# Kernel tuning notes

Measured on AMD Instinct MI355X. Metric: run time of the kernel, lower is better.

Reference implementation:

```python
import jax, jax.numpy as jnp
import numpy as np

M, N, H, C = 50000, 50000, 32, 128
K, GROUPS = 15, 8
CPG = C // GROUPS           # 16, channels per group
RADIUS, SIGMA, INF = 2.5, 1.0, 1.0e6
EPS = 1e-5                  # GroupNorm eps
NEG_SLOPE = 0.1             # LeakyReLU slope in alpha MLP


def setup_inputs() -> dict:
    key = jax.random.key(0)
    ks = jax.random.split(key, 12)
    q_pts = jax.random.normal(ks[0], (M, 3), jnp.float32) * 5.0
    s_pts = q_pts  # same-resolution layer: q == s
    s_feats = jax.random.normal(ks[1], (N, C), jnp.float32)
    neighb_inds = jax.random.randint(ks[2], (M, H), 0, N + 1)  # N = padding index
    # kernel points: center + 14 points in a sphere of given radius
    kp = jax.random.normal(ks[3], (K, 3), jnp.float32)
    kp = kp / (jnp.linalg.norm(kp, axis=1, keepdims=True) + 1e-9) * RADIUS * 0.66
    k_pts = kp.at[0].set(0.0)
    # alpha MLP: Linear(C->C) + LeakyReLU + Linear(C->K*CPG)
    W1 = jax.random.normal(ks[4], (C, C), jnp.float32) * np.sqrt(2.0 / C)
    b1 = jnp.zeros((C,), jnp.float32)
    W2 = jax.random.normal(ks[5], (C, K * CPG), jnp.float32) * np.sqrt(2.0 / C)
    b2 = jnp.zeros((K * CPG,), jnp.float32)
    gn_w = jnp.ones((K * CPG,), jnp.float32)
    gn_b = jnp.zeros((K * CPG,), jnp.float32)
    return {"q_pts": q_pts, "s_pts": s_pts, "s_feats": s_feats,
            "neighb_inds": neighb_inds, "k_pts": k_pts,
            "W1": W1, "b1": b1, "W2": W2, "b2": b2,
            "gn_w": gn_w, "gn_b": gn_b}


def reference(q_pts, s_pts, s_feats, k_pts, W1, b1, W2, b2, gn_w, gn_b, neighb_inds):
    m = q_pts.shape[0]
    # ---- neighbor geometry (no_grad in original) ----
    s_pts_pad = jnp.concatenate([s_pts, jnp.full((1, 3), INF, s_pts.dtype)], 0)
    neighbors = s_pts_pad[neighb_inds] - q_pts[:, None, :]          # (M,H,3)
    sq = jnp.sum((neighbors[:, :, None, :] - k_pts) ** 2, -1)       # (M,H,K)
    nn_sq = jnp.min(sq, -1)                                         # (M,H)
    nn_1nn = jnp.argmin(sq, -1)                                     # (M,H)
    infl = jnp.clip(1.0 - jnp.sqrt(nn_sq) / SIGMA, 0.0)             # linear influence
    # ---- neighbor features gather (padding row = zeros) ----
    feats_pad = jnp.concatenate([s_feats, jnp.zeros((1, C), s_feats.dtype)], 0)
    neighbor_feats = feats_pad[neighb_inds]                         # (M,H,C)
    # ---- dynamic weights from center features (q==s -> pooled = s_feats) ----
    pooled = s_feats
    h = pooled @ W1 + b1
    h = jnp.where(h >= 0, h, NEG_SLOPE * h)                         # LeakyReLU(0.1)
    cw = (h @ W2 + b2).reshape(m, K, CPG)                           # (M,K,CPG)
    # GroupNorm(K groups over K*CPG channels), stats over (points, CPG) per group
    mu = jnp.mean(cw, axis=(0, 2), keepdims=True)
    var = jnp.var(cw, axis=(0, 2), keepdims=True)
    cw = (cw - mu) * jax.lax.rsqrt(var + EPS)
    cw = cw * gn_w.reshape(1, K, CPG) + gn_b.reshape(1, K, CPG)
    # ---- gather weights at nearest kernel point, modulate by influence ----
    nw = jnp.take_along_axis(cw, nn_1nn[:, :, None], axis=1)        # (M,H,CPG)
    nw = nw * infl[:, :, None]                                      # weight_act = identity
    # ---- multiply and sum over neighbors ----
    nf = neighbor_feats.reshape(m, H, CPG, GROUPS)
    out = jnp.sum(nf * nw[:, :, :, None], axis=1)                   # (M,CPG,GROUPS)
    return out.reshape(m, C)
```

## Files before the change

### kernel.cpp

```cpp
#include <hip/hip_runtime.h>
#include <hip/hip_bf16.h>

#define Mpts 50000
#define Npts 50000
#define Hn 32
#define Cc 128
#define Kk 15
#define NCW 240

typedef __attribute__((ext_vector_type(8))) short short8;
typedef __attribute__((ext_vector_type(4))) float f32x4;
typedef __attribute__((ext_vector_type(2))) float f32x2;
typedef unsigned int u32;

__device__ inline ushort f2bf(float f) {
  __hip_bfloat16 h = __float2bfloat16(f);
  return *reinterpret_cast<ushort*>(&h);
}

__global__ __launch_bounds__(256) void k0_pre(
    const float* __restrict__ W1, const float* __restrict__ W2,
    ushort* __restrict__ sfb, ushort* __restrict__ W1t,
    ushort* __restrict__ W2t, float* __restrict__ stats)
{
  __shared__ ushort TT[240][66];
  const int t = threadIdx.x;
  const int b = blockIdx.x;
  if (b < 2) {
    const int k0 = b * 64;
#pragma unroll
    for (int i = 0; i < 32; ++i) {
      int e = t + i * 256;
      int r = e >> 7, c = e & 127;
      TT[c][r] = f2bf(W1[(size_t)(k0 + r) * Cc + c]);
    }
    __syncthreads();
    int n = t >> 1, half = t & 1;
    union { short8 v[4]; ushort u[32]; } pk;
#pragma unroll
    for (int i = 0; i < 32; ++i) pk.u[i] = TT[n][half * 32 + i];
#pragma unroll
    for (int q = 0; q < 4; ++q)
      *(short8*)(W1t + (size_t)n * Cc + k0 + half * 32 + q * 8) = pk.v[q];
  } else if (b < 4) {
    const int k0 = (b - 2) * 64;
    for (int i = 0; i < 60; ++i) {
      int e = t + i * 256;
      int r = e / 240, c = e % 240;
      TT[c][r] = f2bf(W2[(size_t)(k0 + r) * NCW + c]);
    }
    __syncthreads();
    if (t < 240) {
      union { short8 v[8]; ushort u[64]; } pk;
#pragma unroll
      for (int i = 0; i < 64; ++i) pk.u[i] = TT[t][i];
#pragma unroll
      for (int q = 0; q < 8; ++q)
        *(short8*)(W2t + (size_t)t * Cc + k0 + q * 8) = pk.v[q];
    }
  } else {
    if (t < 16) {
      short8 z = short8{0,0,0,0,0,0,0,0};
      *(short8*)(sfb + (size_t)Npts * Cc + t * 8) = z;
    }
    if (t < 128) {
      float4 z4 = make_float4(0.f, 0.f, 0.f, 0.f);
      *(float4*)(stats + t * 4) = z4;
    }
  }
}

__global__ __launch_bounds__(256, 3) void k1_mlp(
    const float* __restrict__ sfeat, const ushort* __restrict__ W1t,
    const float* __restrict__ b1, const ushort* __restrict__ W2t,
    const float* __restrict__ b2, ushort* __restrict__ sfb,
    ushort* __restrict__ cw, float* __restrict__ stats)
{
  __shared__ __align__(16) ushort shA[64 * 128];
  __shared__ __align__(16) ushort shW[128 * 128];
  __shared__ float red[2][15][4];

  const int t = threadIdx.x;
  const int r0 = blockIdx.x * 64;
  const int wid = t >> 6, lane = t & 63;
  const int l16 = lane & 15, lq = lane >> 4;

  float4 fA[4], fB[4];
#pragma unroll
  for (int p = 0; p < 4; ++p) {
    int id = p * 256 + t;
    int r = id >> 4, c = id & 15;
    int g = r0 + r;
    fA[p] = make_float4(0.f, 0.f, 0.f, 0.f);
    fB[p] = make_float4(0.f, 0.f, 0.f, 0.f);
    if (g < Mpts) {
      const float* src = sfeat + (size_t)g * Cc + c * 8;
      fA[p] = *(const float4*)(src);
      fB[p] = *(const float4*)(src + 4);
    }
  }
  uint4 wv[8];
#pragma unroll
  for (int p = 0; p < 8; ++p) {
    int id = p * 256 + t;
    int r = id >> 4, c = id & 15;
    wv[p] = *(const uint4*)(W1t + r * Cc + c * 8);
  }
  asm volatile("" :: "v"(wv[0].x), "v"(wv[1].x), "v"(wv[2].x), "v"(wv[3].x),
                     "v"(wv[4].x), "v"(wv[5].x), "v"(wv[6].x), "v"(wv[7].x),
                     "v"(fA[0].x), "v"(fA[1].x), "v"(fA[2].x), "v"(fA[3].x),
                     "v"(fB[0].x), "v"(fB[1].x), "v"(fB[2].x), "v"(fB[3].x));
#pragma unroll
  for (int p = 0; p < 8; ++p) {
    int id = p * 256 + t;
    int r = id >> 4, c = id & 15;
    *(uint4*)((char*)shW + ((r * 256 + c * 16) ^ ((r & 7) << 4))) = wv[p];
  }
#pragma unroll
  for (int p = 0; p < 4; ++p) {
    int id = p * 256 + t;
    int r = id >> 4, c = id & 15;
    int g = r0 + r;
    union { short8 s; ushort u[8]; } pk;
    pk.u[0] = f2bf(fA[p].x); pk.u[1] = f2bf(fA[p].y); pk.u[2] = f2bf(fA[p].z); pk.u[3] = f2bf(fA[p].w);
    pk.u[4] = f2bf(fB[p].x); pk.u[5] = f2bf(fB[p].y); pk.u[6] = f2bf(fB[p].z); pk.u[7] = f2bf(fB[p].w);
    if (g < Mpts) *(short8*)(sfb + (size_t)g * Cc + c * 8) = pk.s;
    *(short8*)((char*)shA + ((r * 256 + c * 16) ^ ((r & 7) << 4))) = pk.s;
  }
  __syncthreads();

  const int arow = wid * 16 + l16;
  const int axor = (arow & 7) << 4;

  f32x4 acc1[8];
#pragma unroll
  for (int nt = 0; nt < 8; ++nt) acc1[nt] = f32x4{0.f, 0.f, 0.f, 0.f};
#pragma unroll
  for (int kt = 0; kt < 4; ++kt) {
    const int koff2 = (kt * 32 + lq * 8) * 2;
    short8 a = *(const short8*)((const char*)shA + ((arow * 256 + koff2) ^ axor));
#pragma unroll
    for (int nt = 0; nt < 8; ++nt) {
      int wrow = nt * 16 + l16;
      short8 b = *(const short8*)((const char*)shW + ((wrow * 256 + koff2) ^ ((wrow & 7) << 4)));
      acc1[nt] = __builtin_amdgcn_mfma_f32_16x16x32_bf16(a, b, acc1[nt], 0, 0, 0);
    }
  }
#pragma unroll
  for (int nt = 0; nt < 8; ++nt) {
    int col = nt * 16 + l16;
    float bias = b1[col];
#pragma unroll
    for (int reg = 0; reg < 4; ++reg) {
      float h = acc1[nt][reg] + bias;
      h = h >= 0.f ? h : 0.1f * h;
      int row = wid * 16 + lq * 4 + reg;
      int byte = ((row * 256) + col * 2) ^ ((row & 7) << 4);
      *(ushort*)((char*)shA + byte) = f2bf(h);
    }
  }

  f32x4 acc2[8], acc3[7];
#pragma unroll
  for (int j = 0; j < 8; ++j) acc2[j] = f32x4{0.f, 0.f, 0.f, 0.f};
#pragma unroll
  for (int j = 0; j < 7; ++j) acc3[j] = f32x4{0.f, 0.f, 0.f, 0.f};

  __syncthreads();
  {
    uint4 wv2[8];
#pragma unroll
    for (int p = 0; p < 8; ++p) {
      int id = p * 256 + t;
      int r = id >> 4, c = id & 15;
      wv2[p] = *(const uint4*)(W2t + (size_t)r * Cc + c * 8);
    }
    asm volatile("" :: "v"(wv2[0].x), "v"(wv2[1].x), "v"(wv2[2].x), "v"(wv2[3].x),
                       "v"(wv2[4].x), "v"(wv2[5].x), "v"(wv2[6].x), "v"(wv2[7].x));
#pragma unroll
    for (int p = 0; p < 8; ++p) {
      int id = p * 256 + t;
      int r = id >> 4, c = id & 15;
      *(uint4*)((char*)shW + ((r * 256 + c * 16) ^ ((r & 7) << 4))) = wv2[p];
    }
  }
  __syncthreads();
#pragma unroll
  for (int kt = 0; kt < 4; ++kt) {
    const int koff2 = (kt * 32 + lq * 8) * 2;
    short8 a = *(const short8*)((const char*)shA + ((arow * 256 + koff2) ^ axor));
#pragma unroll
    for (int j = 0; j < 8; ++j) {
      int wrow = j * 16 + l16;
      short8 b = *(const short8*)((const char*)shW + ((wrow * 256 + koff2) ^ ((wrow & 7) << 4)));
      acc2[j] = __builtin_amdgcn_mfma_f32_16x16x32_bf16(a, b, acc2[j], 0, 0, 0);
    }
  }

  __syncthreads();
  {
    uint4 wv2[7];
#pragma unroll
    for (int p = 0; p < 7; ++p) {
      int id = p * 256 + t;
      int r = id >> 4, c = id & 15;
      wv2[p] = *(const uint4*)(W2t + (size_t)(128 + r) * Cc + c * 8);
    }
    asm volatile("" :: "v"(wv2[0].x), "v"(wv2[1].x), "v"(wv2[2].x), "v"(wv2[3].x),
                       "v"(wv2[4].x), "v"(wv2[5].x), "v"(wv2[6].x));
#pragma unroll
    for (int p = 0; p < 7; ++p) {
      int id = p * 256 + t;
      int r = id >> 4, c = id & 15;
      *(uint4*)((char*)shW + ((r * 256 + c * 16) ^ ((r & 7) << 4))) = wv2[p];
    }
  }
  __syncthreads();
#pragma unroll
  for (int kt = 0; kt < 4; ++kt) {
    const int koff2 = (kt * 32 + lq * 8) * 2;
    short8 a = *(const short8*)((const char*)shA + ((arow * 256 + koff2) ^ axor));
#pragma unroll
    for (int j = 0; j < 7; ++j) {
      int wrow = j * 16 + l16;
      short8 b = *(const short8*)((const char*)shW + ((wrow * 256 + koff2) ^ ((wrow & 7) << 4)));
      acc3[j] = __builtin_amdgcn_mfma_f32_16x16x32_bf16(a, b, acc3[j], 0, 0, 0);
    }
  }
  __syncthreads();

  ushort* shB = shW;
  float s[15], ss[15];
#pragma unroll
  for (int j = 0; j < 15; ++j) { s[j] = 0.f; ss[j] = 0.f; }
  const int rowb = wid * 16 + lq * 4;
#pragma unroll
  for (int j = 0; j < 15; ++j) {
    int col = j * 16 + l16;
    float bias = b2[col];
#pragma unroll
    for (int reg = 0; reg < 4; ++reg) {
      float v = (j < 8 ? acc2[j][reg] : acc3[j - 8][reg]) + bias;
      shB[(rowb + reg) * 244 + col] = f2bf(v);
      if (r0 + rowb + reg < Mpts) { s[j] += v; ss[j] += v * v; }
    }
  }
  __syncthreads();

  {
    char* cwB = (char*)cw + (size_t)r0 * 480;
#pragma unroll
    for (int i = 0; i < 8; ++i) {
      int gid = i * 256 + t;
      if (gid < 1920) {
        int row = gid / 30;
        int rem = (gid - row * 30) * 16;
        if (r0 + row < Mpts) {
          uint4 v = *(const uint4*)((const char*)shB + row * 488 + rem);
          *(uint4*)(cwB + (size_t)row * 480 + rem) = v;
        }
      }
    }
  }

#pragma unroll
  for (int j = 0; j < 15; ++j) {
    for (int off = 32; off > 0; off >>= 1) {
      s[j]  += __shfl_xor(s[j],  off);
      ss[j] += __shfl_xor(ss[j], off);
    }
  }
  if (lane == 0) {
#pragma unroll
    for (int j = 0; j < 15; ++j) { red[0][j][wid] = s[j]; red[1][j][wid] = ss[j]; }
  }
  __syncthreads();
  float* st = stats + (blockIdx.x & 7) * 64;
  if (t < 15) {
    float S = red[0][t][0] + red[0][t][1] + red[0][t][2] + red[0][t][3];
    atomicAdd(&st[t], S);
  } else if (t >= 32 && t < 47) {
    int j = t - 32;
    float SS = red[1][j][0] + red[1][j][1] + red[1][j][2] + red[1][j][3];
    atomicAdd(&st[32 + j], SS);
  }
}

__global__ __launch_bounds__(256) void k3_out(
    const float* __restrict__ q_pts, const float* __restrict__ s_pts,
    const ushort* __restrict__ sfb, const int* __restrict__ nb,
    const float* __restrict__ kp, const float* __restrict__ gn_w,
    const float* __restrict__ gn_b, const float* __restrict__ stats,
    const ushort* __restrict__ cw, float* __restrict__ out)
{
  __shared__ float Atab[255], Btab[255];
  __shared__ float mus[16], rss[16];
  __shared__ float kpt[3][15];
  __shared__ float wtab[4][2][8][33];
  const int t = threadIdx.x;

  if (t < 15) {
    float S = 0.f, SS = 0.f;
#pragma unroll
    for (int r = 0; r < 8; ++r) { S += stats[r * 64 + t]; SS += stats[r * 64 + 32 + t]; }
    const float inv = 1.0f / (16.0f * (float)Mpts);
    float mu = S * inv;
    float var = SS * inv - mu * mu;
    mus[t] = mu;
    rss[t] = rsqrtf(var + 1e-5f);
  } else if (t >= 64 && t < 109) {
    int i = t - 64;
    kpt[i % 3][i / 3] = kp[i];
  }
  __syncthreads();
  if (t < 240) {
    int k = t >> 4, c = t & 15;
    float a = rss[k] * gn_w[t];
    Atab[k * 17 + c] = a;
    Btab[k * 17 + c] = gn_b[t] - mus[k] * a;
  }
  __syncthreads();

  const int half = (blockIdx.x >= 6250) ? 1 : 0;
  const int pblk = blockIdx.x - half * 6250;
  const int wid = t >> 6, lane = t & 63;
  const int mbase = pblk * 8 + wid * 2;
  const int gtid = pblk * 256 + t;
  const int ch = lane & 7, hlane = (lane >> 3) & 3, p = lane >> 5;
  const int half8 = half * 8;

  int idxv = nb[gtid]; if (idxv > Npts) idxv = Npts;

  int ih[8];
#pragma unroll
  for (int j = 0; j < 8; ++j)
    ih[j] = __shfl(idxv, (p << 5) | (hlane + 4 * j));
  const uint4* fb = (const uint4*)sfb;
  uint4 fv[8];
#pragma unroll
  for (int j = 0; j < 8; ++j)
    fv[j] = fb[ih[j] * 16 + half8 + ch];

  u32 gpk;
  {
    const int mg = mbase + (lane >> 5);
    float qx = q_pts[mg * 3 + 0], qy = q_pts[mg * 3 + 1], qz = q_pts[mg * 3 + 2];
    float px, py, pz;
    if (idxv < Npts) { px = s_pts[idxv * 3 + 0]; py = s_pts[idxv * 3 + 1]; pz = s_pts[idxv * 3 + 2]; }
    else             { px = 1.0e6f; py = 1.0e6f; pz = 1.0e6f; }
    float nx = px - qx, ny = py - qy, nz = pz - qz;
    int ksel = 0; float best = 1e30f;
#pragma unroll
    for (int k = 0; k < Kk; ++k) {
      float dx = nx - kpt[0][k], dy = ny - kpt[1][k], dz = nz - kpt[2][k];
      float d = dx * dx + dy * dy + dz * dz;
      if (d < best) { best = d; ksel = k; }
    }
    float infl = 1.f - sqrtf(best);
    infl = infl > 0.f ? infl : 0.f;
    gpk = (__float_as_uint(infl) & 0xFFFFFFF0u) | (u32)ksel;
  }

  {
    int h = lane >> 1, c0 = (lane & 1) * 4;
#pragma unroll
    for (int q = 0; q < 2; ++q) {
      u32 gp = __shfl((int)gpk, (q << 5) | h);
      int kh = gp & 15;
      float wI = __uint_as_float(gp & 0xFFFFFFF0u);
      uint2 cwv = *(const uint2*)(cw + (size_t)(mbase + q) * NCW + kh * 16 + half8 + c0);
      const float* Ar = &Atab[kh * 17 + half8 + c0];
      const float* Br = &Btab[kh * 17 + half8 + c0];
      float v0 = __uint_as_float(cwv.x << 16);
      float v1 = __uint_as_float(cwv.x & 0xffff0000u);
      float v2 = __uint_as_float(cwv.y << 16);
      float v3 = __uint_as_float(cwv.y & 0xffff0000u);
      wtab[wid][q][c0 + 0][h] = fmaf(v0, Ar[0], Br[0]) * wI;
      wtab[wid][q][c0 + 1][h] = fmaf(v1, Ar[1], Br[1]) * wI;
      wtab[wid][q][c0 + 2][h] = fmaf(v2, Ar[2], Br[2]) * wI;
      wtab[wid][q][c0 + 3][h] = fmaf(v3, Ar[3], Br[3]) * wI;
    }
  }

  asm volatile("" :: "v"(fv[0].x), "v"(fv[1].x), "v"(fv[2].x), "v"(fv[3].x),
                     "v"(fv[4].x), "v"(fv[5].x), "v"(fv[6].x), "v"(fv[7].x));

  f32x2 a0 = {0.f, 0.f}, a1 = {0.f, 0.f}, a2 = {0.f, 0.f}, a3 = {0.f, 0.f};
#pragma unroll
  for (int j = 0; j < 8; ++j) {
    float w = wtab[wid][p][ch][hlane + 4 * j];
    f32x2 w2 = {w, w};
    u32 ux = fv[j].x, uy = fv[j].y, uz = fv[j].z, uw = fv[j].w;
    f32x2 q0 = {__uint_as_float(ux << 16), __uint_as_float(ux & 0xffff0000u)};
    f32x2 q1 = {__uint_as_float(uy << 16), __uint_as_float(uy & 0xffff0000u)};
    f32x2 q2 = {__uint_as_float(uz << 16), __uint_as_float(uz & 0xffff0000u)};
    f32x2 q3 = {__uint_as_float(uw << 16), __uint_as_float(uw & 0xffff0000u)};
    a0 = __builtin_elementwise_fma(q0, w2, a0);
    a1 = __builtin_elementwise_fma(q1, w2, a1);
    a2 = __builtin_elementwise_fma(q2, w2, a2);
    a3 = __builtin_elementwise_fma(q3, w2, a3);
  }
#pragma unroll
  for (int off = 8; off <= 16; off <<= 1) {
    a0[0] += __shfl_xor(a0[0], off); a0[1] += __shfl_xor(a0[1], off);
    a1[0] += __shfl_xor(a1[0], off); a1[1] += __shfl_xor(a1[1], off);
    a2[0] += __shfl_xor(a2[0], off); a2[1] += __shfl_xor(a2[1], off);
    a3[0] += __shfl_xor(a3[0], off); a3[1] += __shfl_xor(a3[1], off);
  }
  if ((lane & 24) == 0) {
    float* op = out + (size_t)(mbase + p) * Cc + half * 64 + ch * 8;
    float4 o0; o0.x = a0[0]; o0.y = a0[1]; o0.z = a1[0]; o0.w = a1[1];
    float4 o1; o1.x = a2[0]; o1.y = a2[1]; o1.z = a3[0]; o1.w = a3[1];
    *(float4*)(op)     = o0;
    *(float4*)(op + 4) = o1;
  }
}

extern "C" void kernel_launch(void* const* d_in, const int* in_sizes, int n_in,
                              void* d_out, int out_size, void* d_ws, size_t ws_size,
                              hipStream_t stream) {
  const float* q_pts  = (const float*)d_in[0];
  const float* s_pts  = (const float*)d_in[1];
  const float* sfeat  = (const float*)d_in[2];
  const int*   nb     = (const int*)d_in[3];
  const float* kp     = (const float*)d_in[4];
  const float* W1     = (const float*)d_in[5];
  const float* b1     = (const float*)d_in[6];
  const float* W2     = (const float*)d_in[7];
  const float* b2     = (const float*)d_in[8];
  const float* gn_w   = (const float*)d_in[9];
  const float* gn_b   = (const float*)d_in[10];
  float* out   = (float*)d_out;

  char* wsb = (char*)d_ws;
  float*  stats = (float*)wsb;
  ushort* sfb   = (ushort*)(wsb + 4096);
  ushort* W1t   = (ushort*)(wsb + 12804352);
  ushort* W2t   = (ushort*)(wsb + 12837120);
  ushort* cwb   = (ushort*)(wsb + 12898560);

  k0_pre<<<5, 256, 0, stream>>>(W1, W2, sfb, W1t, W2t, stats);
  k1_mlp<<<(Mpts + 63) / 64, 256, 0, stream>>>(sfeat, W1t, b1, W2t, b2,
                                               sfb, cwb, stats);
  k3_out<<<12500, 256, 0, stream>>>(q_pts, s_pts, sfb, nb, kp, gn_w, gn_b,
                                    stats, cwb, out);
}
```

Before: 108.6 us.

## Move neighbor geometry computation from output kernel into MLP kernel

The nearest-kernel-point search and influence computation move out of k3_out and into k1_mlp, which writes a packed per-neighbor word (influence plus kernel index) to a workspace buffer. Previously k3_out ran this work twice, once per channel half. The geometry now runs once and overlaps with the MLP kernel's tail, and k3_out only reads one u32 per neighbor. The cost is an extra 6.4 MB write and read through global memory, plus more work in k1_mlp, which may affect its occupancy.

```diff
diff --git a/kernel.cpp b/kernel.cpp
--- a/kernel.cpp
+++ b/kernel.cpp
@@ -74,16 +74,22 @@
     const float* __restrict__ sfeat, const ushort* __restrict__ W1t,
     const float* __restrict__ b1, const ushort* __restrict__ W2t,
     const float* __restrict__ b2, ushort* __restrict__ sfb,
-    ushort* __restrict__ cw, float* __restrict__ stats)
+    ushort* __restrict__ cw, float* __restrict__ stats,
+    const float* __restrict__ q_pts, const float* __restrict__ s_pts,
+    const int* __restrict__ nb, const float* __restrict__ kp,
+    u32* __restrict__ geomP)
 {
   __shared__ __align__(16) ushort shA[64 * 128];
   __shared__ __align__(16) ushort shW[128 * 128];
   __shared__ float red[2][15][4];
+  __shared__ float kptS[45];
 
   const int t = threadIdx.x;
   const int r0 = blockIdx.x * 64;
   const int wid = t >> 6, lane = t & 63;
   const int l16 = lane & 15, lq = lane >> 4;
+
+  if (t < 45) kptS[t] = kp[t];
 
   float4 fA[4], fB[4];
 #pragma unroll
@@ -263,6 +269,33 @@
     }
   }
 
+  {
+    const int gbase = blockIdx.x * 2048 + t;
+#pragma unroll
+    for (int i = 0; i < 8; ++i) {
+      int gt = gbase + i * 256;
+      if (gt < Mpts * Hn) {
+        int idx = nb[gt]; if (idx > Npts) idx = Npts;
+        int m = gt >> 5;
+        float qx = q_pts[m * 3 + 0], qy = q_pts[m * 3 + 1], qz = q_pts[m * 3 + 2];
+        float px, py, pz;
+        if (idx < Npts) { px = s_pts[idx * 3 + 0]; py = s_pts[idx * 3 + 1]; pz = s_pts[idx * 3 + 2]; }
+        else            { px = 1.0e6f; py = 1.0e6f; pz = 1.0e6f; }
+        float nx = px - qx, ny = py - qy, nz = pz - qz;
+        int ksel = 0; float best = 1e30f;
+#pragma unroll
+        for (int k = 0; k < Kk; ++k) {
+          float dx = nx - kptS[k * 3 + 0], dy = ny - kptS[k * 3 + 1], dz = nz - kptS[k * 3 + 2];
+          float d = dx * dx + dy * dy + dz * dz;
+          if (d < best) { best = d; ksel = k; }
+        }
+        float infl = 1.f - sqrtf(best);
+        infl = infl > 0.f ? infl : 0.f;
+        geomP[gt] = (__float_as_uint(infl) & 0xFFFFFFF0u) | (u32)ksel;
+      }
+    }
+  }
+
 #pragma unroll
   for (int j = 0; j < 15; ++j) {
     for (int off = 32; off > 0; off >>= 1) {
@@ -287,15 +320,13 @@
 }
 
 __global__ __launch_bounds__(256) void k3_out(
-    const float* __restrict__ q_pts, const float* __restrict__ s_pts,
     const ushort* __restrict__ sfb, const int* __restrict__ nb,
-    const float* __restrict__ kp, const float* __restrict__ gn_w,
+    const u32* __restrict__ geomP, const float* __restrict__ gn_w,
     const float* __restrict__ gn_b, const float* __restrict__ stats,
     const ushort* __restrict__ cw, float* __restrict__ out)
 {
   __shared__ float Atab[255], Btab[255];
   __shared__ float mus[16], rss[16];
-  __shared__ float kpt[3][15];
   __shared__ float wtab[4][2][8][33];
   const int t = threadIdx.x;
 
@@ -308,9 +339,6 @@
     float var = SS * inv - mu * mu;
     mus[t] = mu;
     rss[t] = rsqrtf(var + 1e-5f);
-  } else if (t >= 64 && t < 109) {
-    int i = t - 64;
-    kpt[i % 3][i / 3] = kp[i];
   }
   __syncthreads();
   if (t < 240) {
@@ -329,43 +357,22 @@
   const int ch = lane & 7, hlane = (lane >> 3) & 3, p = lane >> 5;
   const int half8 = half * 8;
 
+  u32 g = geomP[gtid];
   int idxv = nb[gtid]; if (idxv > Npts) idxv = Npts;
 
-  int ih[8];
-#pragma unroll
-  for (int j = 0; j < 8; ++j)
-    ih[j] = __shfl(idxv, (p << 5) | (hlane + 4 * j));
   const uint4* fb = (const uint4*)sfb;
   uint4 fv[8];
 #pragma unroll
-  for (int j = 0; j < 8; ++j)
-    fv[j] = fb[ih[j] * 16 + half8 + ch];
-
-  u32 gpk;
-  {
-    const int mg = mbase + (lane >> 5);
-    float qx = q_pts[mg * 3 + 0], qy = q_pts[mg * 3 + 1], qz = q_pts[mg * 3 + 2];
-    float px, py, pz;
-    if (idxv < Npts) { px = s_pts[idxv * 3 + 0]; py = s_pts[idxv * 3 + 1]; pz = s_pts[idxv * 3 + 2]; }
-    else             { px = 1.0e6f; py = 1.0e6f; pz = 1.0e6f; }
-    float nx = px - qx, ny = py - qy, nz = pz - qz;
-    int ksel = 0; float best = 1e30f;
-#pragma unroll
-    for (int k = 0; k < Kk; ++k) {
-      float dx = nx - kpt[0][k], dy = ny - kpt[1][k], dz = nz - kpt[2][k];
-      float d = dx * dx + dy * dy + dz * dz;
-      if (d < best) { best = d; ksel = k; }
-    }
-    float infl = 1.f - sqrtf(best);
-    infl = infl > 0.f ? infl : 0.f;
-    gpk = (__float_as_uint(infl) & 0xFFFFFFF0u) | (u32)ksel;
+  for (int j = 0; j < 8; ++j) {
+    int ih = __shfl(idxv, (p << 5) | (hlane + 4 * j));
+    fv[j] = fb[ih * 16 + half8 + ch];
   }
 
   {
     int h = lane >> 1, c0 = (lane & 1) * 4;
 #pragma unroll
     for (int q = 0; q < 2; ++q) {
-      u32 gp = __shfl((int)gpk, (q << 5) | h);
+      u32 gp = __shfl((int)g, (q << 5) | h);
       int kh = gp & 15;
       float wI = __uint_as_float(gp & 0xFFFFFFF0u);
       uint2 cwv = *(const uint2*)(cw + (size_t)(mbase + q) * NCW + kh * 16 + half8 + c0);
@@ -438,10 +445,12 @@
   ushort* W1t   = (ushort*)(wsb + 12804352);
   ushort* W2t   = (ushort*)(wsb + 12837120);
   ushort* cwb   = (ushort*)(wsb + 12898560);
+  u32*    geomP = (u32*)   (wsb + 36898560);
 
   k0_pre<<<5, 256, 0, stream>>>(W1, W2, sfb, W1t, W2t, stats);
   k1_mlp<<<(Mpts + 63) / 64, 256, 0, stream>>>(sfeat, W1t, b1, W2t, b2,
-                                               sfb, cwb, stats);
-  k3_out<<<12500, 256, 0, stream>>>(q_pts, s_pts, sfb, nb, kp, gn_w, gn_b,
-                                    stats, cwb, out);
+                                               sfb, cwb, stats,
+                                               q_pts, s_pts, nb, kp, geomP);
+  k3_out<<<12500, 256, 0, stream>>>(sfb, nb, geomP, gn_w, gn_b, stats,
+                                    cwb, out);
 }
```

Measured after the change: 105.1 us. -3.3%, faster.
